# Performance work log

Measured on AMD Instinct MI355X. Metric: run time of the kernel, lower is better.

## Reference

```python
import jax, jax.numpy as jnp
import numpy as np

DIM = 128
B, NQ, NK = 4, 4096, 4096
SCALE = DIM ** -0.5


def setup_inputs() -> dict:
    key = jax.random.key(0)
    ks = jax.random.split(key, 13)
    def lin(k, shape, scale=0.02):
        return jax.random.normal(k, shape, dtype=jnp.float32) * scale
    return {
        "query": jax.random.normal(ks[0], (B, NQ, DIM), dtype=jnp.float32),
        "key": jax.random.normal(ks[1], (B, NK, DIM), dtype=jnp.float32),
        "value": jax.random.normal(ks[2], (B, NK, DIM), dtype=jnp.float32),
        "att_bias": jax.random.normal(ks[3], (B, NK), dtype=jnp.float32),
        # params, [in, out] layout (torch Linear is x @ W.T + b)
        "q_w": lin(ks[4], (DIM, DIM)), "q_b": jnp.zeros((DIM,), jnp.float32),
        "k_w": lin(ks[5], (DIM, DIM)),
        "v_w": lin(ks[6], (DIM, DIM)), "v_b": jnp.zeros((DIM,), jnp.float32),
        "vs_w": lin(ks[7], (DIM, 1)), "vs_b": jnp.zeros((1,), jnp.float32),
        "p_w": lin(ks[8], (DIM, DIM)), "p_b": jnp.zeros((DIM,), jnp.float32),
    }


def reference(query, key, value, att_bias, q_w, q_b, k_w, v_w, v_b, vs_w, vs_b, p_w, p_b):
    # projections
    q = query @ q_w + q_b                      # [B, NQ, D]
    k = key @ k_w                              # [B, NK, D] (no bias)
    v = value @ v_w + v_b                      # [B, NK, D]
    # per-key semantic scalar, broadcast over queries: [B, 1, NK]
    semantic = (value @ vs_w + vs_b).reshape(value.shape[0], 1, value.shape[1])
    # scores + biases
    attn = jnp.einsum('bqd,bkd->bqk', q, k) * SCALE + semantic
    attn = attn + att_bias[:, None, :]
    attn = jax.nn.softmax(attn, axis=-1)
    out = jnp.einsum('bqk,bkd->bqd', attn, v)  # [B, NQ, D]
    out = out @ p_w + p_b
    return out
```

## Files before the change

### kernel.cpp

```cpp
#include <hip/hip_runtime.h>

typedef __bf16 bf16x8 __attribute__((ext_vector_type(8)));
typedef float f32x4 __attribute__((ext_vector_type(4)));
typedef float f32x16 __attribute__((ext_vector_type(16)));

#define MFMA16(a,b,c) __builtin_amdgcn_mfma_f32_16x16x32_bf16(a,b,c,0,0,0)
#define MFMA32(a,b,c) __builtin_amdgcn_mfma_f32_32x32x16_bf16(a,b,c,0,0,0)

static __device__ __forceinline__ unsigned short f2bf(float f){
  union{float f;unsigned u;}v; v.f=f;
  unsigned u=v.u;
  u += 0x7fffu + ((u>>16)&1u);
  return (unsigned short)(u>>16);
}
static __device__ __forceinline__ float bf2f(unsigned short h){
  union{unsigned u;float f;}v; v.u=((unsigned)h)<<16; return v.f;
}
static __device__ __forceinline__ unsigned cvtpk(float lo, float hi){
  unsigned r;
  asm("v_cvt_pk_bf16_f32 %0, %1, %2" : "=v"(r) : "v"(lo), "v"(hi));
  return r;
}
static __device__ __forceinline__ void gload16(const void* g, void* l){
  __builtin_amdgcn_global_load_lds(
    (const __attribute__((address_space(1))) unsigned int*)(uintptr_t)g,
    (__attribute__((address_space(3))) unsigned int*)(uintptr_t)l,
    16, 0, 0);
}

#define SCALE_QK 0.08838834764831845f
#define LOG2E    1.44269504088896340f
#define M0_L2    16.0f

#define NSPLIT   6

#define SWZ128(r,c) (((r)<<7) + ((c) ^ (((r)&7)<<3)))


__global__ __launch_bounds__(256) void k_proj(
    const float* __restrict__ query, const float* __restrict__ key,
    const float* __restrict__ value, const float* __restrict__ att_bias,
    const float* __restrict__ q_w, const float* __restrict__ q_b,
    const float* __restrict__ k_w, const float* __restrict__ v_w,
    const float* __restrict__ v_b, const float* __restrict__ vs_w,
    const float* __restrict__ vs_b,
    unsigned short* __restrict__ qp, unsigned short* __restrict__ kp,
    unsigned short* __restrict__ vpt, float* __restrict__ biasc)
{
  const int t = blockIdx.y;
  const float* X = (t==0) ? query : ((t==1) ? key : value);
  const float* W = (t==0) ? q_w  : ((t==1) ? k_w : v_w);
  const int tid = threadIdx.x;
  const int row0 = blockIdx.x * 64;

  __shared__ __align__(16) unsigned short Wt[128][136];
  __shared__ __align__(16) unsigned short Xs[64][136];
  __shared__ float vsw_s[128];

  #pragma unroll 4
  for (int i=0;i<16;i++){
    int idx = tid*64 + i*4;
    float4 v4 = *(const float4*)(W + idx);
    Wt[(idx+0)&127][(idx+0)>>7] = f2bf(v4.x);
    Wt[(idx+1)&127][(idx+1)>>7] = f2bf(v4.y);
    Wt[(idx+2)&127][(idx+2)>>7] = f2bf(v4.z);
    Wt[(idx+3)&127][(idx+3)>>7] = f2bf(v4.w);
  }
  {
    const float* Xb = X + (size_t)row0*128;
    #pragma unroll
    for (int i=0;i<8;i++){
      int f4 = i*256 + tid;
      int row = f4>>5, c4 = f4&31;
      float4 v = *(const float4*)(Xb + row*128 + c4*4);
      ushort4 h;
      h.x = f2bf(v.x); h.y = f2bf(v.y); h.z = f2bf(v.z); h.w = f2bf(v.w);
      *(ushort4*)&Xs[row][c4*4] = h;
    }
  }
  if (t==2 && tid<128) vsw_s[tid] = vs_w[tid];
  __syncthreads();

  const int w = tid>>6, lane = tid&63, lr = lane&15, lg = lane>>4;
  f32x4 acc[8];
  #pragma unroll
  for (int nt=0;nt<8;nt++) acc[nt] = (f32x4){0.f,0.f,0.f,0.f};
  #pragma unroll
  for (int kk=0;kk<4;kk++){
    bf16x8 a = *(const bf16x8*)&Xs[w*16+lr][kk*32+lg*8];
    #pragma unroll
    for (int nt=0;nt<8;nt++){
      bf16x8 bb = *(const bf16x8*)&Wt[nt*16+lr][kk*32+lg*8];
      acc[nt] = MFMA16(a,bb,acc[nt]);
    }
  }

  if (t < 2){
    const float* bias = (t==0) ? q_b : (const float*)nullptr;
    const float sc = (t==0) ? (SCALE_QK*LOG2E) : 1.f;
    unsigned short* dstm = (t==0) ? qp : kp;
    #pragma unroll
    for (int nt=0;nt<8;nt++){
      int col = nt*16+lr;
      float bv = bias ? bias[col] : 0.f;
      #pragma unroll
      for (int r=0;r<4;r++){
        int row = row0 + w*16 + lg*4 + r;
        dstm[(size_t)row*128+col] = f2bf((acc[nt][r] + bv) * sc);
      }
    }
  } else {
    {
      int rl = tid>>2, part = tid&3;
      float s = 0.f;
      #pragma unroll
      for (int j=0;j<32;j++){
        int d = part*32+j;
        s += bf2f(Xs[rl][d]) * vsw_s[d];
      }
      s += __shfl_xor(s,1);
      s += __shfl_xor(s,2);
      if ((tid&3)==0){
        int rg = row0 + rl;
        biasc[rg] = (s + vs_b[0] + att_bias[rg]) * LOG2E - M0_L2;
      }
    }
    __syncthreads();
    unsigned short* Vls = (unsigned short*)Wt;
    #pragma unroll
    for (int nt=0;nt<8;nt++){
      int col = nt*16+lr;
      float bv = v_b[col];
      #pragma unroll
      for (int r=0;r<4;r++){
        int rl_ = w*16 + lg*4 + r;
        int k5 = rl_ & 31;
        int pos = 16*(k5>>4) + (k5&3) + 4*((k5>>3)&1) + 8*((k5>>2)&1);
        int np = (rl_ & 32) | pos;
        Vls[col*72 + np] = f2bf(acc[nt][r] + bv);
      }
    }
    __syncthreads();
    int d = tid>>1, half = tid&1;
    int bi = row0>>12, n0 = row0&4095;
    unsigned short* dst = vpt + ((size_t)(bi*128+d))*4096 + n0 + half*32;
    const unsigned short* src = Vls + d*72 + half*32;
    #pragma unroll
    for (int i=0;i<4;i++)
      *(uint4*)(dst + i*8) = *(const uint4*)(src + i*8);
  }
}

__global__ __launch_bounds__(256,3) void k_flash(
    const unsigned short* __restrict__ qp, const unsigned short* __restrict__ kp,
    const unsigned short* __restrict__ vpt, const float* __restrict__ biasc,
    unsigned short* __restrict__ opart, float* __restrict__ ml)
{
  const int f = blockIdx.x;
  const int xcd = f & 7, slot = f >> 3;
  const int group = xcd*3 + (slot>>5);
  const int b = group/NSPLIT, split = group%NSPLIT;
  const int q0 = (slot & 31) * 128;
  const int ts = 21*split + (split<2 ? split : 2);
  const int nt = (split<2) ? 22 : 21;

  const int tid = threadIdx.x;
  const int w = tid>>6, lane = tid&63;
  const int l31 = lane&31, hi = lane>>5;

  __shared__ __align__(16) unsigned short Ks[3][32*128];
  __shared__ __align__(16) char Vp[3][8192];
  __shared__ __align__(16) float Bs[768];

  const unsigned short* kbase = kp  + (size_t)(b*4096 + ts*32)*128;
  const char* vbase = (const char*)(vpt + (size_t)b*128*4096 + ts*32);
  const float* bbase = biasc + b*4096 + ts*32;

  if (w < 3) gload16(bbase + w*256 + lane*4, (char*)Bs + w*1024);

  bf16x8 qf[8];
  {
    const unsigned short* qrow = qp + ((size_t)(b*4096 + q0 + w*32 + l31))*128;
    #pragma unroll
    for (int kk=0;kk<8;kk++) qf[kk] = *(const bf16x8*)(qrow + kk*16 + hi*8);
  }

  #define STAGE(bf_, k0_) do{                                                 \
    const char* kb_ = (const char*)kbase + (size_t)(k0_)*256;                 \
    const char* vb_ = vbase + (size_t)(k0_)*2;                                \
    _Pragma("unroll")                                                         \
    for (int i=0;i<2;i++){                                                    \
      int s_ = w*2+i;                                                         \
      int kr = s_*4 + (lane>>4);                                              \
      gload16(kb_ + kr*256 + (((lane&15)*16) ^ ((kr&7)*16)),                  \
              (char*)Ks[bf_] + s_*1024);                                      \
      int u_ = (lane&7) ^ ((lane>>3)&7);                                      \
      int vd = s_*16 + ((lane>>3)<<1) + (u_>>2);                              \
      gload16(vb_ + (size_t)vd*8192 + ((u_&3)<<4),                            \
              (char*)Vp[bf_] + s_*1024);                                      \
    }                                                                         \
  }while(0)

  float l_run = 0.f;
  f32x16 acc[4];
  #pragma unroll
  for (int dt=0;dt<4;dt++) acc[dt] = (f32x16){};

  STAGE(0, 0);
  STAGE(1, 32);

  const int vA = (l31>>1)*128;
  const int vX = ((l31>>1)&7)<<4;
  const int vH = (l31&1)*64 + hi*16;

  int cur = 0;
  for (int t=0;t<nt;t++){
    if (t < nt-1) asm volatile("s_waitcnt vmcnt(4)" ::: "memory");
    else          asm volatile("s_waitcnt vmcnt(0)" ::: "memory");
    __builtin_amdgcn_s_barrier();
    __builtin_amdgcn_sched_barrier(0);

    if (t+2 < nt){
      int b2 = cur+2; if (b2>=3) b2-=3;
      STAGE(b2, (t+2)*32);
    }

    const unsigned short* Kc = Ks[cur];
    const char* Vc = Vp[cur];

    const float* Bt = &Bs[t*32];
    float4 b0 = *(const float4*)&Bt[hi*4];
    float4 b1 = *(const float4*)&Bt[8 + hi*4];
    float4 b2v = *(const float4*)&Bt[16 + hi*4];
    float4 b3 = *(const float4*)&Bt[24 + hi*4];
    f32x16 sc;
    sc[0]=b0.x;  sc[1]=b0.y;  sc[2]=b0.z;  sc[3]=b0.w;
    sc[4]=b1.x;  sc[5]=b1.y;  sc[6]=b1.z;  sc[7]=b1.w;
    sc[8]=b2v.x; sc[9]=b2v.y; sc[10]=b2v.z; sc[11]=b2v.w;
    sc[12]=b3.x; sc[13]=b3.y; sc[14]=b3.z; sc[15]=b3.w;

    __builtin_amdgcn_s_setprio(1);
    #pragma unroll
    for (int kk=0;kk<8;kk++){
      bf16x8 a = *(const bf16x8*)&Kc[SWZ128(l31, kk*16 + hi*8)];
      sc = MFMA32(a, qf[kk], sc);
    }
    __builtin_amdgcn_s_setprio(0);

    float rs = 0.f;
    #pragma unroll
    for (int i=0;i<16;i++){
      sc[i] = __builtin_exp2f(sc[i]); rs += sc[i];
    }
    rs += __shfl_xor(rs, 32);
    l_run += rs;

    {
      union { unsigned u[4]; bf16x8 v; } pu0;
      pu0.u[0] = cvtpk(sc[0], sc[1]);
      pu0.u[1] = cvtpk(sc[2], sc[3]);
      pu0.u[2] = cvtpk(sc[4], sc[5]);
      pu0.u[3] = cvtpk(sc[6], sc[7]);
      __builtin_amdgcn_s_setprio(1);
      #pragma unroll
      for (int dt=0;dt<4;dt++){
        bf16x8 v0 = *(const bf16x8*)(Vc + dt*2048 + vA + ((vH +  0) ^ vX));
        acc[dt] = MFMA32(pu0.v, v0, acc[dt]);
      }
      __builtin_amdgcn_s_setprio(0);
    }
    {
      union { unsigned u[4]; bf16x8 v; } pu1;
      pu1.u[0] = cvtpk(sc[8],  sc[9]);
      pu1.u[1] = cvtpk(sc[10], sc[11]);
      pu1.u[2] = cvtpk(sc[12], sc[13]);
      pu1.u[3] = cvtpk(sc[14], sc[15]);
      __builtin_amdgcn_s_setprio(1);
      #pragma unroll
      for (int dt=0;dt<4;dt++){
        bf16x8 v1 = *(const bf16x8*)(Vc + dt*2048 + vA + ((vH + 32) ^ vX));
        acc[dt] = MFMA32(pu1.v, v1, acc[dt]);
      }
      __builtin_amdgcn_s_setprio(0);
    }

    cur = (cur+1 == 3) ? 0 : cur+1;
  }
  #undef STAGE

  const size_t rowbase = (size_t)split*16384 + (size_t)b*4096 + q0;
  #pragma unroll
  for (int r=0;r<16;r++){
    int qn = (r&3) + 8*(r>>2) + 4*hi;
    float inv = 1.f/__shfl(l_run, qn);
    size_t row = rowbase + w*32 + qn;
    opart[row*128 +      l31] = f2bf(acc[0][r]*inv);
    opart[row*128 + 32 + l31] = f2bf(acc[1][r]*inv);
    opart[row*128 + 64 + l31] = f2bf(acc[2][r]*inv);
    opart[row*128 + 96 + l31] = f2bf(acc[3][r]*inv);
  }
  if (hi==0){
    size_t rg = rowbase + w*32 + l31;
    ml[rg*2]   = 0.f;
    ml[rg*2+1] = l_run;
  }
}

__global__ __launch_bounds__(256) void k_outproj(
    const unsigned short* __restrict__ opart, const float* __restrict__ ml,
    const float* __restrict__ p_w, const float* __restrict__ p_b,
    float* __restrict__ out)
{
  const int tid = threadIdx.x;
  const int row0 = blockIdx.x*32;
  __shared__ __align__(16) unsigned short Wt[128][136];
  __shared__ __align__(16) unsigned short Xs[32][136];
  __shared__ float wmg[NSPLIT][32];

  #pragma unroll 4
  for (int i=0;i<16;i++){
    int idx = tid*64 + i*4;
    float4 v4 = *(const float4*)(p_w + idx);
    Wt[(idx+0)&127][(idx+0)>>7] = f2bf(v4.x);
    Wt[(idx+1)&127][(idx+1)>>7] = f2bf(v4.y);
    Wt[(idx+2)&127][(idx+2)>>7] = f2bf(v4.z);
    Wt[(idx+3)&127][(idx+3)>>7] = f2bf(v4.w);
  }
  if (tid < 32){
    int row = row0 + tid;
    float l[NSPLIT], wsum = 0.f;
    #pragma unroll
    for (int i=0;i<NSPLIT;i++){
      l[i] = ml[((size_t)i*16384 + row)*2 + 1];
      wsum += l[i];
    }
    float inv = 1.f/wsum;
    #pragma unroll
    for (int i=0;i<NSPLIT;i++) wmg[i][tid] = l[i]*inv;
  }
  __syncthreads();
  #pragma unroll
  for (int i=0;i<2;i++){
    int e = (i*256 + tid)*8;
    int row = e>>7, col = e&127;
    float a8[8];
    #pragma unroll
    for (int j=0;j<8;j++) a8[j] = 0.f;
    #pragma unroll
    for (int s=0;s<NSPLIT;s++){
      uint4 v = *(const uint4*)(opart + ((size_t)s*16384 + row0 + row)*128 + col);
      float wv = wmg[s][row];
      const unsigned short* hp = (const unsigned short*)&v;
      #pragma unroll
      for (int j=0;j<8;j++) a8[j] += wv * bf2f(hp[j]);
    }
    unsigned short h8[8];
    #pragma unroll
    for (int j=0;j<8;j++) h8[j] = f2bf(a8[j]);
    *(uint4*)&Xs[row][col] = *(const uint4*)h8;
  }
  __syncthreads();

  const int w=tid>>6, lane=tid&63, lr=lane&15, lg=lane>>4;
  const int r0 = (w&1)*16, c0 = (w>>1)*64;
  f32x4 acc[4];
  #pragma unroll
  for (int nt=0;nt<4;nt++) acc[nt] = (f32x4){0.f,0.f,0.f,0.f};
  #pragma unroll
  for (int kk=0;kk<4;kk++){
    bf16x8 a = *(const bf16x8*)&Xs[r0+lr][kk*32+lg*8];
    #pragma unroll
    for (int nt=0;nt<4;nt++){
      bf16x8 bb = *(const bf16x8*)&Wt[c0+nt*16+lr][kk*32+lg*8];
      acc[nt] = MFMA16(a,bb,acc[nt]);
    }
  }
  __syncthreads();
  float* Os = (float*)Wt;
  #pragma unroll
  for (int nt=0;nt<4;nt++){
    int col = c0 + nt*16 + lr;
    float pb = p_b[col];
    #pragma unroll
    for (int r=0;r<4;r++){
      int row = r0 + lg*4 + r;
      Os[row*132 + col] = acc[nt][r] + pb;
    }
  }
  __syncthreads();
  {
    int row = tid>>3, seg = tid&7;
    const float* src = Os + row*132 + seg*16;
    float* dst = out + (size_t)(row0+row)*128 + seg*16;
    #pragma unroll
    for (int i=0;i<4;i++)
      *(float4*)(dst + i*4) = *(const float4*)(src + i*4);
  }
}

extern "C" void kernel_launch(void* const* d_in, const int* in_sizes, int n_in,
                              void* d_out, int out_size, void* d_ws, size_t ws_size,
                              hipStream_t stream) {
  (void)in_sizes; (void)n_in; (void)out_size; (void)ws_size;
  const float* query    = (const float*)d_in[0];
  const float* key      = (const float*)d_in[1];
  const float* value    = (const float*)d_in[2];
  const float* att_bias = (const float*)d_in[3];
  const float* q_w = (const float*)d_in[4];
  const float* q_b = (const float*)d_in[5];
  const float* k_w = (const float*)d_in[6];
  const float* v_w = (const float*)d_in[7];
  const float* v_b = (const float*)d_in[8];
  const float* vs_w = (const float*)d_in[9];
  const float* vs_b = (const float*)d_in[10];
  const float* p_w = (const float*)d_in[11];
  const float* p_b = (const float*)d_in[12];

  char* ws = (char*)d_ws;
  unsigned short* qp    = (unsigned short*)(ws);
  unsigned short* kp    = (unsigned short*)(ws + 4194304);
  unsigned short* vpt   = (unsigned short*)(ws + 8388608);
  float*          biasc = (float*)(ws + 12582912);
  unsigned short* opart = (unsigned short*)(ws + 12648448);
  float*          ml    = (float*)(ws + 46202880);

  hipLaunchKernelGGL(k_proj, dim3(256,3), dim3(256), 0, stream,
    query,key,value,att_bias,q_w,q_b,k_w,v_w,v_b,vs_w,vs_b,qp,kp,vpt,biasc);
  hipLaunchKernelGGL(k_flash, dim3(768), dim3(256), 0, stream,
    qp,kp,vpt,biasc,opart,ml);
  hipLaunchKernelGGL(k_outproj, dim3(512), dim3(256), 0, stream,
    opart,ml,p_w,p_b,(float*)d_out);
}
```

Measured before the change: 75.37 us.

## Software-pipeline QK scores one tile ahead and interleave with PV MFMAs

Restructures the attention inner loop so the QK^T MFMA for tile t+1 is issued interleaved with the PV MFMAs for tile t, while the exp/convert for tile t runs before the barrier. This is meant to hide the softmax exp latency and the serial dependency between score computation and PV accumulation behind MFMA work. In exchange it keeps two score tiles live, which raises register pressure. It also changes the wait to vmcnt(0) each iteration, which may reduce how far global loads overlap with compute.

```diff
diff --git a/kernel.cpp b/kernel.cpp
--- a/kernel.cpp
+++ b/kernel.cpp
@@ -201,6 +201,18 @@
     }                                                                         \
   }while(0)
 
+  #define BIAS_INIT(dst_, tt_) do{                                            \
+    const float* Bt_ = &Bs[(tt_)*32];                                         \
+    float4 c0_ = *(const float4*)&Bt_[hi*4];                                  \
+    float4 c1_ = *(const float4*)&Bt_[8 + hi*4];                              \
+    float4 c2_ = *(const float4*)&Bt_[16 + hi*4];                             \
+    float4 c3_ = *(const float4*)&Bt_[24 + hi*4];                             \
+    dst_[0]=c0_.x;  dst_[1]=c0_.y;  dst_[2]=c0_.z;  dst_[3]=c0_.w;            \
+    dst_[4]=c1_.x;  dst_[5]=c1_.y;  dst_[6]=c1_.z;  dst_[7]=c1_.w;            \
+    dst_[8]=c2_.x;  dst_[9]=c2_.y;  dst_[10]=c2_.z; dst_[11]=c2_.w;           \
+    dst_[12]=c3_.x; dst_[13]=c3_.y; dst_[14]=c3_.z; dst_[15]=c3_.w;           \
+  }while(0)
+
   float l_run = 0.f;
   f32x16 acc[4];
   #pragma unroll
@@ -213,10 +225,38 @@
   const int vX = ((l31>>1)&7)<<4;
   const int vH = (l31&1)*64 + hi*16;
 
+  asm volatile("s_waitcnt vmcnt(4)" ::: "memory");
+  __builtin_amdgcn_s_barrier();
+  __builtin_amdgcn_sched_barrier(0);
+
+  f32x16 sc_cur;
+  BIAS_INIT(sc_cur, 0);
+  #pragma unroll
+  for (int kk=0;kk<8;kk++){
+    bf16x8 a = *(const bf16x8*)&Ks[0][SWZ128(l31, kk*16 + hi*8)];
+    sc_cur = MFMA32(a, qf[kk], sc_cur);
+  }
+
   int cur = 0;
-  for (int t=0;t<nt;t++){
-    if (t < nt-1) asm volatile("s_waitcnt vmcnt(4)" ::: "memory");
-    else          asm volatile("s_waitcnt vmcnt(0)" ::: "memory");
+  for (int t=0;t<nt-1;t++){
+    float rs = 0.f;
+    #pragma unroll
+    for (int i=0;i<16;i++){
+      sc_cur[i] = __builtin_exp2f(sc_cur[i]); rs += sc_cur[i];
+    }
+    rs += __shfl_xor(rs, 32);
+    l_run += rs;
+    union { unsigned u[4]; bf16x8 v; } pu0, pu1;
+    pu0.u[0] = cvtpk(sc_cur[0],  sc_cur[1]);
+    pu0.u[1] = cvtpk(sc_cur[2],  sc_cur[3]);
+    pu0.u[2] = cvtpk(sc_cur[4],  sc_cur[5]);
+    pu0.u[3] = cvtpk(sc_cur[6],  sc_cur[7]);
+    pu1.u[0] = cvtpk(sc_cur[8],  sc_cur[9]);
+    pu1.u[1] = cvtpk(sc_cur[10], sc_cur[11]);
+    pu1.u[2] = cvtpk(sc_cur[12], sc_cur[13]);
+    pu1.u[3] = cvtpk(sc_cur[14], sc_cur[15]);
+
+    asm volatile("s_waitcnt vmcnt(0)" ::: "memory");
     __builtin_amdgcn_s_barrier();
     __builtin_amdgcn_sched_barrier(0);
 
@@ -225,68 +265,57 @@
       STAGE(b2, (t+2)*32);
     }
 
-    const unsigned short* Kc = Ks[cur];
+    int nxt = cur+1; if (nxt>=3) nxt-=3;
+    const unsigned short* Kn = Ks[nxt];
     const char* Vc = Vp[cur];
 
-    const float* Bt = &Bs[t*32];
-    float4 b0 = *(const float4*)&Bt[hi*4];
-    float4 b1 = *(const float4*)&Bt[8 + hi*4];
-    float4 b2v = *(const float4*)&Bt[16 + hi*4];
-    float4 b3 = *(const float4*)&Bt[24 + hi*4];
-    f32x16 sc;
-    sc[0]=b0.x;  sc[1]=b0.y;  sc[2]=b0.z;  sc[3]=b0.w;
-    sc[4]=b1.x;  sc[5]=b1.y;  sc[6]=b1.z;  sc[7]=b1.w;
-    sc[8]=b2v.x; sc[9]=b2v.y; sc[10]=b2v.z; sc[11]=b2v.w;
-    sc[12]=b3.x; sc[13]=b3.y; sc[14]=b3.z; sc[15]=b3.w;
+    f32x16 sc_next;
+    BIAS_INIT(sc_next, t+1);
 
     __builtin_amdgcn_s_setprio(1);
     #pragma unroll
     for (int kk=0;kk<8;kk++){
-      bf16x8 a = *(const bf16x8*)&Kc[SWZ128(l31, kk*16 + hi*8)];
-      sc = MFMA32(a, qf[kk], sc);
+      bf16x8 a = *(const bf16x8*)&Kn[SWZ128(l31, kk*16 + hi*8)];
+      sc_next = MFMA32(a, qf[kk], sc_next);
+      const int dt = kk&3, hf = kk>>2;
+      bf16x8 v = *(const bf16x8*)(Vc + dt*2048 + vA + ((vH + hf*32) ^ vX));
+      acc[dt] = MFMA32(hf ? pu1.v : pu0.v, v, acc[dt]);
     }
     __builtin_amdgcn_s_setprio(0);
 
+    sc_cur = sc_next;
+    cur = nxt;
+  }
+
+  {
     float rs = 0.f;
     #pragma unroll
     for (int i=0;i<16;i++){
-      sc[i] = __builtin_exp2f(sc[i]); rs += sc[i];
+      sc_cur[i] = __builtin_exp2f(sc_cur[i]); rs += sc_cur[i];
     }
     rs += __shfl_xor(rs, 32);
     l_run += rs;
-
-    {
-      union { unsigned u[4]; bf16x8 v; } pu0;
-      pu0.u[0] = cvtpk(sc[0], sc[1]);
-      pu0.u[1] = cvtpk(sc[2], sc[3]);
-      pu0.u[2] = cvtpk(sc[4], sc[5]);
-      pu0.u[3] = cvtpk(sc[6], sc[7]);
-      __builtin_amdgcn_s_setprio(1);
-      #pragma unroll
-      for (int dt=0;dt<4;dt++){
-        bf16x8 v0 = *(const bf16x8*)(Vc + dt*2048 + vA + ((vH +  0) ^ vX));
-        acc[dt] = MFMA32(pu0.v, v0, acc[dt]);
-      }
-      __builtin_amdgcn_s_setprio(0);
-    }
-    {
-      union { unsigned u[4]; bf16x8 v; } pu1;
-      pu1.u[0] = cvtpk(sc[8],  sc[9]);
-      pu1.u[1] = cvtpk(sc[10], sc[11]);
-      pu1.u[2] = cvtpk(sc[12], sc[13]);
-      pu1.u[3] = cvtpk(sc[14], sc[15]);
-      __builtin_amdgcn_s_setprio(1);
-      #pragma unroll
-      for (int dt=0;dt<4;dt++){
-        bf16x8 v1 = *(const bf16x8*)(Vc + dt*2048 + vA + ((vH + 32) ^ vX));
-        acc[dt] = MFMA32(pu1.v, v1, acc[dt]);
-      }
-      __builtin_amdgcn_s_setprio(0);
-    }
-
-    cur = (cur+1 == 3) ? 0 : cur+1;
+    union { unsigned u[4]; bf16x8 v; } pu0, pu1;
+    pu0.u[0] = cvtpk(sc_cur[0],  sc_cur[1]);
+    pu0.u[1] = cvtpk(sc_cur[2],  sc_cur[3]);
+    pu0.u[2] = cvtpk(sc_cur[4],  sc_cur[5]);
+    pu0.u[3] = cvtpk(sc_cur[6],  sc_cur[7]);
+    pu1.u[0] = cvtpk(sc_cur[8],  sc_cur[9]);
+    pu1.u[1] = cvtpk(sc_cur[10], sc_cur[11]);
+    pu1.u[2] = cvtpk(sc_cur[12], sc_cur[13]);
+    pu1.u[3] = cvtpk(sc_cur[14], sc_cur[15]);
+    const char* Vc = Vp[cur];
+    __builtin_amdgcn_s_setprio(1);
+    #pragma unroll
+    for (int kk=0;kk<8;kk++){
+      const int dt = kk&3, hf = kk>>2;
+      bf16x8 v = *(const bf16x8*)(Vc + dt*2048 + vA + ((vH + hf*32) ^ vX));
+      acc[dt] = MFMA32(hf ? pu1.v : pu0.v, v, acc[dt]);
+    }
+    __builtin_amdgcn_s_setprio(0);
   }
   #undef STAGE
+  #undef BIAS_INIT
 
   const size_t rowbase = (size_t)split*16384 + (size_t)b*4096 + q0;
   #pragma unroll
```

New measurement: 74.61 us, median of 2. Within noise of the previous version (-1.0%).
